# Performance work log

Hardware: AMD Instinct MI355X
Metric: run time of the kernel (lower is better)

The kernel has to match this reference:

```python
import jax, jax.numpy as jnp
import numpy as np

B, T, C = 2, 2048, 768
N_HEADS = 12
HEAD = C // N_HEADS


def setup_inputs() -> dict:
    key = jax.random.key(0)
    k1, k2, k3 = jax.random.split(key, 3)
    x = jax.random.normal(k1, (B, T, C), dtype=jnp.float32)
    # torch Linear weights: [out_features, in_features]
    W_attn = jax.random.normal(k2, (3 * C, C), dtype=jnp.float32) * 0.02
    W_proj = jax.random.normal(k3, (C, C), dtype=jnp.float32) * 0.02
    return {"x": x, "W_attn": W_attn, "W_proj": W_proj}


def reference(x, W_attn, W_proj):
    b, t, c = x.shape
    qkv = jnp.einsum('btc,oc->bto', x, W_attn)  # [B,T,3C]
    q, k, v = jnp.split(qkv, 3, axis=-1)
    # [B, H, T, D]
    q = q.reshape(b, t, N_HEADS, HEAD).transpose(0, 2, 1, 3)
    k = k.reshape(b, t, N_HEADS, HEAD).transpose(0, 2, 1, 3)
    v = v.reshape(b, t, N_HEADS, HEAD).transpose(0, 2, 1, 3)
    scale = 1.0 / jnp.sqrt(jnp.asarray(HEAD, dtype=x.dtype))
    wei = jnp.einsum('bhqd,bhkd->bhqk', q, k) * scale  # [B,H,T,T]
    causal = jnp.tril(jnp.ones((t, t), dtype=bool))
    wei = jnp.where(causal[None, None], wei, jnp.asarray(-jnp.inf, dtype=wei.dtype))
    wei = jax.nn.softmax(wei, axis=-1)  # dropout p=0 -> identity
    out = jnp.einsum('bhqk,bhkd->bhqd', wei, v)
    out = out.transpose(0, 2, 1, 3).reshape(b, t, c)
    out = jnp.einsum('btc,oc->bto', out, W_proj)
    return out
```

## Files before the change

### kernel.cpp

```cpp
#include <hip/hip_runtime.h>

#define T_DIM 2048
#define C_DIM 768
#define NH    12
#define HD    64
#define KDIM  768
#define JOBS_PER_XCD 96

typedef __attribute__((ext_vector_type(8))) short short8;
typedef __attribute__((ext_vector_type(4))) float f32x4;
typedef unsigned short u16;

__device__ __forceinline__ u16 f2bf(float f) {
    unsigned int u = __builtin_bit_cast(unsigned int, f);
    u = (u + 0x7fffu + ((u >> 16) & 1u)) >> 16;
    return (u16)u;
}
__device__ __forceinline__ unsigned int cvtpk(float a, float b) {
    unsigned int r;
    asm("v_cvt_pk_bf16_f32 %0, %1, %2" : "=v"(r) : "v"(a), "v"(b));
    return r;
}
__device__ __forceinline__ void gload16(const u16* g, u16* l) {
    __builtin_amdgcn_global_load_lds(
        (const __attribute__((address_space(1))) unsigned int*)g,
        (__attribute__((address_space(3))) unsigned int*)l, 16, 0, 0);
}

#define NX  (4096 * 768)
#define NWA (2304 * 768)
#define NWP (768 * 768)
#define TOT4 ((NX + NWA + NWP) / 4)

__global__ __launch_bounds__(256) void convert_all(
    const float* __restrict__ x, const float* __restrict__ wa,
    const float* __restrict__ wp, u16* __restrict__ xb,
    u16* __restrict__ wab, u16* __restrict__ wpb, int* __restrict__ counters)
{
    if (blockIdx.x == 0 && threadIdx.x < 8) counters[threadIdx.x * 16] = 0;
    for (int i4 = blockIdx.x * 256 + threadIdx.x; i4 < TOT4; i4 += gridDim.x * 256) {
        int i = i4 * 4;
        const float* src; u16* dst; int off;
        if (i < NX)            { src = x;  dst = xb;  off = i; }
        else if (i < NX + NWA) { src = wa; dst = wab; off = i - NX; }
        else                   { src = wp; dst = wpb; off = i - NX - NWA; }
        float4 v = *(const float4*)&src[off];
        ushort4 o;
        o.x = f2bf(v.x); o.y = f2bf(v.y); o.z = f2bf(v.z); o.w = f2bf(v.w);
        *(ushort4*)&dst[off] = o;
    }
}

__global__ __launch_bounds__(256) void gemm_qkv(
    const u16* __restrict__ A, const u16* __restrict__ Wt,
    u16* __restrict__ qb, u16* __restrict__ kb, u16* __restrict__ vtb)
{
    __shared__ __align__(16) u16 AsL[2][128][32];
    __shared__ __align__(16) u16 BsL[2][128][32];

    const int tid = threadIdx.x;
    const int orig = blockIdx.x;
    const int wg = (orig & 7) * 72 + (orig >> 3);
    const int bm = (wg / 18) * 128;
    const int bn = (wg % 18) * 128;

    const int w = tid >> 6, l = tid & 63;
    const int wr = (w >> 1) * 64, wc = (w & 1) * 64;
    const int lrow = l & 15, lg = l >> 4;
    const int lr4 = l >> 2, lc4 = l & 3;

    f32x4 acc[4][4];
    const f32x4 zero4 = {0.f, 0.f, 0.f, 0.f};
#pragma unroll
    for (int mi = 0; mi < 4; ++mi)
#pragma unroll
        for (int ni = 0; ni < 4; ++ni) acc[mi][ni] = zero4;

    auto STAGE = [&](int buf, int k0) {
#pragma unroll
        for (int i = 0; i < 2; ++i) {
            const int rb = w * 32 + i * 16;
            const int row = rb + lr4;
            const int sc = (lc4 ^ (row & 3)) * 8;
            gload16(&A [(size_t)(bm + row) * KDIM + k0 + sc], &AsL[buf][rb][0]);
            gload16(&Wt[(size_t)(bn + row) * KDIM + k0 + sc], &BsL[buf][rb][0]);
        }
    };

    int cur = 0;
    STAGE(0, 0);
    for (int k0 = 0; k0 < KDIM; k0 += 32) {
        __syncthreads();
        if (k0 + 32 < KDIM) STAGE(cur ^ 1, k0 + 32);

        short8 af[4], bf[4];
#pragma unroll
        for (int mi = 0; mi < 4; ++mi)
            af[mi] = *(const short8*)&AsL[cur][wr + mi * 16 + lrow][(lg ^ (lrow & 3)) * 8];
#pragma unroll
        for (int ni = 0; ni < 4; ++ni)
            bf[ni] = *(const short8*)&BsL[cur][wc + ni * 16 + lrow][(lg ^ (lrow & 3)) * 8];
#pragma unroll
        for (int mi = 0; mi < 4; ++mi)
#pragma unroll
            for (int ni = 0; ni < 4; ++ni)
                acc[mi][ni] = __builtin_amdgcn_mfma_f32_16x16x32_bf16(
                    af[mi], bf[ni], acc[mi][ni], 0, 0, 0);
        cur ^= 1;
    }

#pragma unroll
    for (int ni = 0; ni < 4; ++ni) {
        const int colbase = bn + wc + ni * 16;
        const int which = colbase / C_DIM;
        const int h = (colbase % C_DIM) / HD;
        const int d = (colbase % HD) + lrow;
        const float qs = (which == 0) ? 0.18033688011112042f : 1.0f;
#pragma unroll
        for (int mi = 0; mi < 4; ++mi) {
            const int t0 = bm + wr + mi * 16 + lg * 4;
            const int bb2 = t0 >> 11, tt = t0 & 2047;
            const size_t bhoff = (size_t)(bb2 * NH + h);
            if (which == 2) {
                ushort4 pv;
                pv.x = f2bf(acc[mi][ni][0]); pv.y = f2bf(acc[mi][ni][1]);
                pv.z = f2bf(acc[mi][ni][2]); pv.w = f2bf(acc[mi][ni][3]);
                *(ushort4*)&vtb[(bhoff * HD + d) * T_DIM + tt] = pv;
            } else {
                u16* dst = (which == 0) ? qb : kb;
#pragma unroll
                for (int jj = 0; jj < 4; ++jj)
                    dst[(bhoff * T_DIM + tt + jj) * HD + d] = f2bf(acc[mi][ni][jj] * qs);
            }
        }
    }
}

__global__ __launch_bounds__(256) void gemm_proj(
    const u16* __restrict__ A, const u16* __restrict__ Wt,
    float* __restrict__ dense)
{
    __shared__ __align__(16) u16 As[64][40];
    __shared__ __align__(16) u16 Bs[128][40];

    const int tid = threadIdx.x;
    const int orig = blockIdx.x;
    const int wg = (orig & 7) * 48 + (orig >> 3);
    const int bm = (wg / 6) * 64, bn = (wg % 6) * 128;

    const int w = tid >> 6, l = tid & 63;
    const int wr = (w >> 1) * 32, wc = (w & 1) * 64;
    const int lrow = l & 15, lg = l >> 4;

    const int srow = tid >> 2;
    const int scol = (tid & 3) * 8;

    f32x4 acc[2][4];
    const f32x4 zero4 = {0.f, 0.f, 0.f, 0.f};
#pragma unroll
    for (int mi = 0; mi < 2; ++mi)
#pragma unroll
        for (int ni = 0; ni < 4; ++ni) acc[mi][ni] = zero4;

    uint4 ra0 = *(const uint4*)&A [(size_t)(bm + srow)      * KDIM + scol];
    uint4 rb0 = *(const uint4*)&Wt[(size_t)(bn + srow)      * KDIM + scol];
    uint4 rb1 = *(const uint4*)&Wt[(size_t)(bn + 64 + srow) * KDIM + scol];

    for (int k0 = 0; k0 < KDIM; k0 += 32) {
        __syncthreads();
        *(uint4*)&As[srow][scol]      = ra0;
        *(uint4*)&Bs[srow][scol]      = rb0;
        *(uint4*)&Bs[64 + srow][scol] = rb1;
        __syncthreads();

        if (k0 + 32 < KDIM) {
            ra0 = *(const uint4*)&A [(size_t)(bm + srow)      * KDIM + k0 + 32 + scol];
            rb0 = *(const uint4*)&Wt[(size_t)(bn + srow)      * KDIM + k0 + 32 + scol];
            rb1 = *(const uint4*)&Wt[(size_t)(bn + 64 + srow) * KDIM + k0 + 32 + scol];
        }

        short8 af[2], bf[4];
#pragma unroll
        for (int mi = 0; mi < 2; ++mi)
            af[mi] = *(const short8*)&As[wr + mi * 16 + lrow][lg * 8];
#pragma unroll
        for (int ni = 0; ni < 4; ++ni)
            bf[ni] = *(const short8*)&Bs[wc + ni * 16 + lrow][lg * 8];
#pragma unroll
        for (int mi = 0; mi < 2; ++mi)
#pragma unroll
            for (int ni = 0; ni < 4; ++ni)
                acc[mi][ni] = __builtin_amdgcn_mfma_f32_16x16x32_bf16(
                    af[mi], bf[ni], acc[mi][ni], 0, 0, 0);
    }

#pragma unroll
    for (int ni = 0; ni < 4; ++ni) {
        const int col = bn + wc + ni * 16 + lrow;
#pragma unroll
        for (int mi = 0; mi < 2; ++mi) {
            const int m0 = bm + wr + mi * 16 + lg * 4;
#pragma unroll
            for (int jj = 0; jj < 4; ++jj)
                dense[(size_t)(m0 + jj) * C_DIM + col] = acc[mi][ni][jj];
        }
    }
}

__global__ __launch_bounds__(256, 2) void attn_mfma(
    const u16* __restrict__ q, const u16* __restrict__ k,
    const u16* __restrict__ vt, u16* __restrict__ aw, int* __restrict__ counters)
{
    __shared__ __align__(16) u16 KsL [2][128][64];
    __shared__ __align__(16) u16 VtsL[2][64][128];
    __shared__ __align__(16) u16 Ps  [4][16][72];
    __shared__ int job_s;

    const int tid = threadIdx.x, w = tid >> 6, l = tid & 63;
    const int lrow = l & 15, lg = l >> 4;
    const int lr8 = l >> 3, lc8 = l & 7;
    const int lr16 = l >> 4, lc16 = l & 15;
    const int xcdi = blockIdx.x & 7;
    const f32x4 zero4 = {0.f, 0.f, 0.f, 0.f};

    for (;;) {
        __syncthreads();
        if (tid == 0) job_s = atomicAdd(&counters[xcdi * 16], 1);
        __syncthreads();
        const int j = job_s;
        if (j >= JOBS_PER_XCD) break;

        const int qt = 31 - (j / 3);
        const int bh = xcdi * 3 + (j - (j / 3) * 3);
        const int bb = bh / NH, hh = bh % NH;
        const int qbase = qt * 64 + w * 16;
        const int qg = qbase + lrow;

        const u16* Qp = q  + (size_t)bh * T_DIM * HD;
        const u16* Kp = k  + (size_t)bh * T_DIM * HD;
        const u16* Vp = vt + (size_t)bh * HD * T_DIM;

        const short8 aq0 = *(const short8*)&Qp[(size_t)(qbase + lrow) * HD + lg * 8];
        const short8 aq1 = *(const short8*)&Qp[(size_t)(qbase + lrow) * HD + 32 + lg * 8];

        f32x4 o[4];
#pragma unroll
        for (int n = 0; n < 4; ++n) o[n] = zero4;
        float l_run = 0.0f;

        auto STAGE = [&](int buf, int kk0) {
#pragma unroll
            for (int i = 0; i < 4; ++i) {
                const int rb = w * 32 + i * 8;
                const int row = rb + lr8;
                gload16(&Kp[(size_t)(kk0 + row) * HD + ((lc8 ^ (row & 7)) * 8)],
                        &KsL[buf][rb][0]);
            }
#pragma unroll
            for (int i = 0; i < 4; ++i) {
                const int db = w * 16 + i * 4;
                const int d = db + lr16;
                gload16(&Vp[(size_t)d * T_DIM + kk0 + ((lc16 ^ (d & 15)) * 8)],
                        &VtsL[buf][db][0]);
            }
        };

        auto PROCESS = [&](f32x4* s, int sub, int kk0, bool masked) {
            if (masked) {
#pragma unroll
                for (int n = 0; n < 4; ++n)
#pragma unroll
                    for (int jj = 0; jj < 4; ++jj)
                        if (kk0 + sub * 64 + n * 16 + lg * 4 + jj > qg)
                            s[n][jj] = -3.0e38f;
            }
#pragma unroll
            for (int n = 0; n < 4; ++n)
#pragma unroll
                for (int jj = 0; jj < 4; ++jj)
                    s[n][jj] = exp2f(s[n][jj]);
            f32x4 a2 = (s[0] + s[1]) + (s[2] + s[3]);
            l_run += (a2[0] + a2[1]) + (a2[2] + a2[3]);
#pragma unroll
            for (int n = 0; n < 4; ++n) {
                uint2 pr;
                pr.x = cvtpk(s[n][0], s[n][1]);
                pr.y = cvtpk(s[n][2], s[n][3]);
                *(uint2*)&Ps[w][lrow][n * 16 + lg * 4] = pr;
            }
            const short8 ap0 = *(const short8*)&Ps[w][lrow][lg * 8];
            const short8 ap1 = *(const short8*)&Ps[w][lrow][32 + lg * 8];
            const int cur = (kk0 >> 7) & 1;
#pragma unroll
            for (int n = 0; n < 4; ++n) {
                const int row = n * 16 + lrow;
                const short8 bv0 = *(const short8*)
                    &VtsL[cur][row][((sub * 8 + lg) ^ lrow) * 8];
                const short8 bv1 = *(const short8*)
                    &VtsL[cur][row][((sub * 8 + 4 + lg) ^ lrow) * 8];
                o[n] = __builtin_amdgcn_mfma_f32_16x16x32_bf16(ap0, bv0, o[n], 0, 0, 0);
                o[n] = __builtin_amdgcn_mfma_f32_16x16x32_bf16(ap1, bv1, o[n], 0, 0, 0);
            }
        };

        const int nkt = qt / 2 + 1;
        int cur = 0;
        STAGE(0, 0);
        for (int kt = 0; kt < nkt; ++kt) {
            const int kk0 = kt * 128;

            __builtin_amdgcn_s_barrier();

            if (kt + 1 < nkt) {
                STAGE(cur ^ 1, kk0 + 128);
                asm volatile("s_waitcnt vmcnt(8)" ::: "memory");
            } else {
                asm volatile("s_waitcnt vmcnt(0)" ::: "memory");
            }
            __builtin_amdgcn_sched_barrier(0);
            __builtin_amdgcn_s_barrier();

            const bool last = (kt == nkt - 1);
            const int nsub = (last && (qt & 1) == 0) ? 1 : 2;

            f32x4 s0[4], s1[4];
#pragma unroll
            for (int n = 0; n < 4; ++n) {
                const int row = n * 16 + lrow;
                const short8 kf0 = *(const short8*)&KsL[cur][row][((lg)     ^ (lrow & 7)) * 8];
                const short8 kf1 = *(const short8*)&KsL[cur][row][((lg + 4) ^ (lrow & 7)) * 8];
                s0[n] = __builtin_amdgcn_mfma_f32_16x16x32_bf16(kf0, aq0, zero4, 0, 0, 0);
                s0[n] = __builtin_amdgcn_mfma_f32_16x16x32_bf16(kf1, aq1, s0[n], 0, 0, 0);
            }
            if (nsub == 2) {
#pragma unroll
                for (int n = 0; n < 4; ++n) {
                    const int row = 64 + n * 16 + lrow;
                    const short8 kf0 = *(const short8*)&KsL[cur][row][((lg)     ^ (lrow & 7)) * 8];
                    const short8 kf1 = *(const short8*)&KsL[cur][row][((lg + 4) ^ (lrow & 7)) * 8];
                    s1[n] = __builtin_amdgcn_mfma_f32_16x16x32_bf16(kf0, aq0, zero4, 0, 0, 0);
                    s1[n] = __builtin_amdgcn_mfma_f32_16x16x32_bf16(kf1, aq1, s1[n], 0, 0, 0);
                }
            }

            PROCESS(s0, 0, kk0, last && nsub == 1);
            if (nsub == 2) PROCESS(s1, 1, kk0, last);

            cur ^= 1;
        }

        float rs = l_run;
        rs += __shfl_xor(rs, 16);
        rs += __shfl_xor(rs, 32);
#pragma unroll
        for (int jj = 0; jj < 4; ++jj) {
            const float lj = __shfl(rs, lg * 4 + jj);
            const float inv = 1.0f / lj;
            const size_t m = (size_t)bb * T_DIM + qbase + lg * 4 + jj;
#pragma unroll
            for (int n = 0; n < 4; ++n)
                aw[m * C_DIM + hh * HD + n * 16 + lrow] = f2bf(o[n][jj] * inv);
        }
    }
}

extern "C" void kernel_launch(void* const* d_in, const int* in_sizes, int n_in,
                              void* d_out, int out_size, void* d_ws, size_t ws_size,
                              hipStream_t stream) {
    const float* x      = (const float*)d_in[0];
    const float* W_attn = (const float*)d_in[1];
    const float* W_proj = (const float*)d_in[2];
    float* out = (float*)d_out;

    char* ws = (char*)d_ws;
    u16* xb  = (u16*)ws;                       ws += (size_t)NX * 2;
    u16* wab = (u16*)ws;                       ws += (size_t)NWA * 2;
    u16* wpb = (u16*)ws;                       ws += (size_t)NWP * 2;
    u16* qb  = (u16*)ws;                       ws += (size_t)24 * T_DIM * HD * 2;
    u16* kb  = (u16*)ws;                       ws += (size_t)24 * T_DIM * HD * 2;
    u16* vtb = (u16*)ws;                       ws += (size_t)24 * T_DIM * HD * 2;
    u16* awb = (u16*)ws;                       ws += (size_t)4096 * C_DIM * 2;
    int* cnt = (int*)ws;

    convert_all<<<2048, 256, 0, stream>>>(x, W_attn, W_proj, xb, wab, wpb, cnt);

    gemm_qkv<<<576, 256, 0, stream>>>(xb, wab, qb, kb, vtb);

    attn_mfma<<<512, 256, 0, stream>>>(qb, kb, vtb, awb, cnt);

    gemm_proj<<<384, 256, 0, stream>>>(awb, wpb, out);
}
```

Before: 85.94 us.

## Fuse x bf16 conversion into QKV GEMM and async-stage proj GEMM tiles

The separate fp32-to-bf16 pass over x is removed. The QKV GEMM now reads fp32 x into registers, packs it to bf16 with v_cvt_pk_bf16_f32, and writes swizzled LDS tiles, while weight tiles still use global_load_lds. Separately, the projection GEMM switches from register-staged single-buffered LDS to double-buffered direct global-to-LDS loads with XOR swizzle. The fusion avoids writing and re-reading a bf16 copy of x, at the cost of each QKV block re-reading fp32 x across 18 column tiles and adding an extra barrier per k-step.

```diff
diff --git a/kernel.cpp b/kernel.cpp
--- a/kernel.cpp
+++ b/kernel.cpp
@@ -21,29 +21,30 @@
     asm("v_cvt_pk_bf16_f32 %0, %1, %2" : "=v"(r) : "v"(a), "v"(b));
     return r;
 }
+__device__ __forceinline__ uint4 pack8(float4 a, float4 b) {
+    return make_uint4(cvtpk(a.x, a.y), cvtpk(a.z, a.w),
+                      cvtpk(b.x, b.y), cvtpk(b.z, b.w));
+}
 __device__ __forceinline__ void gload16(const u16* g, u16* l) {
     __builtin_amdgcn_global_load_lds(
         (const __attribute__((address_space(1))) unsigned int*)g,
         (__attribute__((address_space(3))) unsigned int*)l, 16, 0, 0);
 }
 
-#define NX  (4096 * 768)
 #define NWA (2304 * 768)
 #define NWP (768 * 768)
-#define TOT4 ((NX + NWA + NWP) / 4)
-
-__global__ __launch_bounds__(256) void convert_all(
-    const float* __restrict__ x, const float* __restrict__ wa,
-    const float* __restrict__ wp, u16* __restrict__ xb,
+#define NWTOT ((NWA + NWP) / 4)
+
+__global__ __launch_bounds__(256) void convert_w(
+    const float* __restrict__ wa, const float* __restrict__ wp,
     u16* __restrict__ wab, u16* __restrict__ wpb, int* __restrict__ counters)
 {
     if (blockIdx.x == 0 && threadIdx.x < 8) counters[threadIdx.x * 16] = 0;
-    for (int i4 = blockIdx.x * 256 + threadIdx.x; i4 < TOT4; i4 += gridDim.x * 256) {
+    for (int i4 = blockIdx.x * 256 + threadIdx.x; i4 < NWTOT; i4 += gridDim.x * 256) {
         int i = i4 * 4;
         const float* src; u16* dst; int off;
-        if (i < NX)            { src = x;  dst = xb;  off = i; }
-        else if (i < NX + NWA) { src = wa; dst = wab; off = i - NX; }
-        else                   { src = wp; dst = wpb; off = i - NX - NWA; }
+        if (i < NWA) { src = wa; dst = wab; off = i; }
+        else         { src = wp; dst = wpb; off = i - NWA; }
         float4 v = *(const float4*)&src[off];
         ushort4 o;
         o.x = f2bf(v.x); o.y = f2bf(v.y); o.z = f2bf(v.z); o.w = f2bf(v.w);
@@ -52,7 +53,7 @@
 }
 
 __global__ __launch_bounds__(256) void gemm_qkv(
-    const u16* __restrict__ A, const u16* __restrict__ Wt,
+    const float* __restrict__ X, const u16* __restrict__ Wt,
     u16* __restrict__ qb, u16* __restrict__ kb, u16* __restrict__ vtb)
 {
     __shared__ __align__(16) u16 AsL[2][128][32];
@@ -69,6 +70,10 @@
     const int lrow = l & 15, lg = l >> 4;
     const int lr4 = l >> 2, lc4 = l & 3;
 
+    const int arow = tid >> 2;
+    const int ac   = tid & 3;
+    const int asw  = (ac ^ (arow & 3)) * 8;
+
     f32x4 acc[4][4];
     const f32x4 zero4 = {0.f, 0.f, 0.f, 0.f};
 #pragma unroll
@@ -76,22 +81,37 @@
 #pragma unroll
         for (int ni = 0; ni < 4; ++ni) acc[mi][ni] = zero4;
 
-    auto STAGE = [&](int buf, int k0) {
+    auto LOADA = [&](int k0, float4* r) {
+        const size_t r0 = (size_t)(bm + arow) * KDIM + k0 + ac * 8;
+        const size_t r1 = (size_t)(bm + 64 + arow) * KDIM + k0 + ac * 8;
+        r[0] = *(const float4*)&X[r0];
+        r[1] = *(const float4*)&X[r0 + 4];
+        r[2] = *(const float4*)&X[r1];
+        r[3] = *(const float4*)&X[r1 + 4];
+    };
+    auto STAGEW = [&](int buf, int k0) {
 #pragma unroll
         for (int i = 0; i < 2; ++i) {
             const int rb = w * 32 + i * 16;
             const int row = rb + lr4;
             const int sc = (lc4 ^ (row & 3)) * 8;
-            gload16(&A [(size_t)(bm + row) * KDIM + k0 + sc], &AsL[buf][rb][0]);
             gload16(&Wt[(size_t)(bn + row) * KDIM + k0 + sc], &BsL[buf][rb][0]);
         }
     };
 
+    float4 ar[4];
+    LOADA(0, ar);
+    STAGEW(0, 0);
     int cur = 0;
-    STAGE(0, 0);
     for (int k0 = 0; k0 < KDIM; k0 += 32) {
         __syncthreads();
-        if (k0 + 32 < KDIM) STAGE(cur ^ 1, k0 + 32);
+        *(uint4*)&AsL[cur][arow][asw]      = pack8(ar[0], ar[1]);
+        *(uint4*)&AsL[cur][64 + arow][asw] = pack8(ar[2], ar[3]);
+        __syncthreads();
+        if (k0 + 32 < KDIM) {
+            LOADA(k0 + 32, ar);
+            STAGEW(cur ^ 1, k0 + 32);
+        }
 
         short8 af[4], bf[4];
 #pragma unroll
@@ -140,8 +160,8 @@
     const u16* __restrict__ A, const u16* __restrict__ Wt,
     float* __restrict__ dense)
 {
-    __shared__ __align__(16) u16 As[64][40];
-    __shared__ __align__(16) u16 Bs[128][40];
+    __shared__ __align__(16) u16 AsL[2][64][32];
+    __shared__ __align__(16) u16 BsL[2][128][32];
 
     const int tid = threadIdx.x;
     const int orig = blockIdx.x;
@@ -151,9 +171,7 @@
     const int w = tid >> 6, l = tid & 63;
     const int wr = (w >> 1) * 32, wc = (w & 1) * 64;
     const int lrow = l & 15, lg = l >> 4;
-
-    const int srow = tid >> 2;
-    const int scol = (tid & 3) * 8;
+    const int lr4 = l >> 2, lc4 = l & 3;
 
     f32x4 acc[2][4];
     const f32x4 zero4 = {0.f, 0.f, 0.f, 0.f};
@@ -162,36 +180,42 @@
 #pragma unroll
         for (int ni = 0; ni < 4; ++ni) acc[mi][ni] = zero4;
 
-    uint4 ra0 = *(const uint4*)&A [(size_t)(bm + srow)      * KDIM + scol];
-    uint4 rb0 = *(const uint4*)&Wt[(size_t)(bn + srow)      * KDIM + scol];
-    uint4 rb1 = *(const uint4*)&Wt[(size_t)(bn + 64 + srow) * KDIM + scol];
-
+    auto STAGE = [&](int buf, int k0) {
+        {
+            const int rb = w * 16;
+            const int row = rb + lr4;
+            const int sc = (lc4 ^ (row & 3)) * 8;
+            gload16(&A[(size_t)(bm + row) * KDIM + k0 + sc], &AsL[buf][rb][0]);
+        }
+#pragma unroll
+        for (int i = 0; i < 2; ++i) {
+            const int rb = w * 32 + i * 16;
+            const int row = rb + lr4;
+            const int sc = (lc4 ^ (row & 3)) * 8;
+            gload16(&Wt[(size_t)(bn + row) * KDIM + k0 + sc], &BsL[buf][rb][0]);
+        }
+    };
+
+    int cur = 0;
+    STAGE(0, 0);
     for (int k0 = 0; k0 < KDIM; k0 += 32) {
         __syncthreads();
-        *(uint4*)&As[srow][scol]      = ra0;
-        *(uint4*)&Bs[srow][scol]      = rb0;
-        *(uint4*)&Bs[64 + srow][scol] = rb1;
-        __syncthreads();
-
-        if (k0 + 32 < KDIM) {
-            ra0 = *(const uint4*)&A [(size_t)(bm + srow)      * KDIM + k0 + 32 + scol];
-            rb0 = *(const uint4*)&Wt[(size_t)(bn + srow)      * KDIM + k0 + 32 + scol];
-            rb1 = *(const uint4*)&Wt[(size_t)(bn + 64 + srow) * KDIM + k0 + 32 + scol];
-        }
+        if (k0 + 32 < KDIM) STAGE(cur ^ 1, k0 + 32);
 
         short8 af[2], bf[4];
 #pragma unroll
         for (int mi = 0; mi < 2; ++mi)
-            af[mi] = *(const short8*)&As[wr + mi * 16 + lrow][lg * 8];
+            af[mi] = *(const short8*)&AsL[cur][wr + mi * 16 + lrow][(lg ^ (lrow & 3)) * 8];
 #pragma unroll
         for (int ni = 0; ni < 4; ++ni)
-            bf[ni] = *(const short8*)&Bs[wc + ni * 16 + lrow][lg * 8];
+            bf[ni] = *(const short8*)&BsL[cur][wc + ni * 16 + lrow][(lg ^ (lrow & 3)) * 8];
 #pragma unroll
         for (int mi = 0; mi < 2; ++mi)
 #pragma unroll
             for (int ni = 0; ni < 4; ++ni)
                 acc[mi][ni] = __builtin_amdgcn_mfma_f32_16x16x32_bf16(
                     af[mi], bf[ni], acc[mi][ni], 0, 0, 0);
+        cur ^= 1;
     }
 
 #pragma unroll
@@ -373,7 +397,6 @@
     float* out = (float*)d_out;
 
     char* ws = (char*)d_ws;
-    u16* xb  = (u16*)ws;                       ws += (size_t)NX * 2;
     u16* wab = (u16*)ws;                       ws += (size_t)NWA * 2;
     u16* wpb = (u16*)ws;                       ws += (size_t)NWP * 2;
     u16* qb  = (u16*)ws;                       ws += (size_t)24 * T_DIM * HD * 2;
@@ -382,9 +405,9 @@
     u16* awb = (u16*)ws;                       ws += (size_t)4096 * C_DIM * 2;
     int* cnt = (int*)ws;
 
-    convert_all<<<2048, 256, 0, stream>>>(x, W_attn, W_proj, xb, wab, wpb, cnt);
-
-    gemm_qkv<<<576, 256, 0, stream>>>(xb, wab, qb, kb, vtb);
+    convert_w<<<512, 256, 0, stream>>>(W_attn, W_proj, wab, wpb, cnt);
+
+    gemm_qkv<<<576, 256, 0, stream>>>(x, wab, qb, kb, vtb);
 
     attn_mfma<<<512, 256, 0, stream>>>(qb, kb, vtb, awb, cnt);
 
```

Measured after the change: 105.5 us. 1.23x slower.
